# Kernel tuning notes

Hardware: AMD Instinct MI355X
Metric: run time of the kernel (lower is better)

Reference implementation:

```python
import jax, jax.numpy as jnp
import numpy as np

B, S, D, H = 4, 1024, 1024, 16
DH = D // H
K_SPARSE = 32
LAMBDA_MAX, ALPHA = 10.0, 5.0
SPARSE_THRESHOLD = 1.0


def setup_inputs() -> dict:
    key = jax.random.key(0)
    ks = jax.random.split(key, 12)
    x = jax.random.normal(ks[0], (B, S, D), dtype=jnp.float32)
    prior_mask = jax.random.bernoulli(ks[1], 0.1, (S, S))
    prior_indices = jax.random.randint(ks[2], (S, K_SPARSE), 0, S)
    prior_index_mask = jax.random.bernoulli(ks[3], 0.9, (S, K_SPARSE))
    prior_index_mask = prior_index_mask.at[:, 0].set(True)  # avoid all-masked rows
    u_prev = jax.random.normal(ks[4], (B, 1), dtype=jnp.float32)
    sc = 1.0 / np.sqrt(D)
    Wq = jax.random.normal(ks[5], (D, D), dtype=jnp.float32) * sc
    Wk = jax.random.normal(ks[6], (D, D), dtype=jnp.float32) * sc
    Wv = jax.random.normal(ks[7], (D, D), dtype=jnp.float32) * sc
    Wo = jax.random.normal(ks[8], (D, D), dtype=jnp.float32) * sc
    bq = jnp.zeros((D,), jnp.float32)
    bk = jnp.zeros((D,), jnp.float32)
    bv = jnp.zeros((D,), jnp.float32)
    bo = jnp.zeros((D,), jnp.float32)
    return {"x": x, "prior_mask": prior_mask, "prior_indices": prior_indices,
            "prior_index_mask": prior_index_mask, "u_prev": u_prev,
            "Wq": Wq, "bq": bq, "Wk": Wk, "bk": bk, "Wv": Wv, "bv": bv,
            "Wo": Wo, "bo": bo}


def reference(x, prior_mask, prior_indices, prior_index_mask, u_prev,
              Wq, bq, Wk, bk, Wv, bv, Wo, bo):
    Bb, Ss, Dd = x.shape
    scale = 1.0 / jnp.sqrt(jnp.asarray(DH, x.dtype))

    def proj(W, b):
        return (x @ W.T + b).reshape(Bb, Ss, H, DH).transpose(0, 2, 1, 3)  # [B,H,S,DH]

    Q, K, V = proj(Wq, bq), proj(Wk, bk), proj(Wv, bv)

    lam = LAMBDA_MAX * jnp.exp(-ALPHA * u_prev.reshape(Bb))  # [B]
    use_sparse = lam >= SPARSE_THRESHOLD                      # [B] bool

    # ---- dense branch: full SDPA with lambda-scaled prior bias ----
    scores = jnp.einsum('bhqd,bhkd->bhqk', Q, K) * scale      # [B,H,S,S]
    prior_bias = jnp.where(prior_mask[:Ss, :Ss], 0.0, -1.0).astype(x.dtype)
    bias = lam[:, None, None, None] * prior_bias[None, None]
    dense_out = jnp.einsum('bhqk,bhkd->bhqd',
                           jax.nn.softmax(scores + bias, axis=-1), V)

    # ---- sparse branch: gather-indexed SDPA over prior_indices ----
    idx = prior_indices[:Ss]                                   # [S,k]
    Kg = K[:, :, idx]                                          # [B,H,S,k,DH]
    Vg = V[:, :, idx]
    s_scores = jnp.einsum('bhsd,bhskd->bhsk', Q, Kg) * scale   # [B,H,S,k]
    s_scores = jnp.where(prior_index_mask[:Ss][None, None], s_scores,
                         jnp.asarray(-jnp.inf, x.dtype))
    sparse_out = jnp.einsum('bhsk,bhskd->bhsd',
                            jax.nn.softmax(s_scores, axis=-1), Vg)

    out = jnp.where(use_sparse[:, None, None, None], sparse_out, dense_out)
    out = out.transpose(0, 2, 1, 3).reshape(Bb, Ss, Dd)
    return out @ Wo.T + bo
```

## Files before the change

### kernel.cpp

```cpp
#include <hip/hip_runtime.h>
#include <hip/hip_bf16.h>
#include <cmath>

#define NB 4
#define NS 1024
#define ND 1024
#define NH 16
#define NDH 64
#define NKSP 32
#define SCALE 0.125f
#define LOG2E 1.44269504f
#define SCALE2 (SCALE * LOG2E)

typedef __attribute__((ext_vector_type(8))) short bf16x8;
typedef __attribute__((ext_vector_type(4))) float f32x4;
typedef unsigned long long u64;

#define AS1 __attribute__((address_space(1)))
#define AS3 __attribute__((address_space(3)))

__device__ __forceinline__ void gl_lds16(const void* g, void* l) {
    __builtin_amdgcn_global_load_lds((const AS1 void*)g, (AS3 void*)l, 16, 0, 0);
}

__device__ __forceinline__ ushort f2bf(float f) {
    union { __hip_bfloat16 h; ushort u; } cv;
    cv.h = __float2bfloat16(f);
    return cv.u;
}
__device__ __forceinline__ float bf2f(ushort u) {
    union { unsigned int i; float f; } cv;
    cv.i = ((unsigned int)u) << 16;
    return cv.f;
}
__device__ __forceinline__ float fexp2(float x) {
    return __builtin_amdgcn_exp2f(x);
}

__global__ __launch_bounds__(256)
void f2bf_multi(const float* __restrict__ x,
                const float* __restrict__ w0, const float* __restrict__ w1,
                const float* __restrict__ w2, const float* __restrict__ w3,
                const int* __restrict__ pm,
                ushort* __restrict__ xo,
                ushort* __restrict__ o0, ushort* __restrict__ o1,
                ushort* __restrict__ o2, ushort* __restrict__ o3,
                u64* __restrict__ bm)
{
    int y = blockIdx.y;
    if (y == 5) {
        int word = blockIdx.x * 4 + (threadIdx.x >> 6);
        int lane = threadIdx.x & 63;
        int row  = word >> 4, wcol = word & 15;
        int v = pm[(size_t)row * NS + wcol * 64 + lane];
        u64 b = __ballot(v != 0);
        if (lane == 0) bm[word] = b;
        return;
    }
    const float* src; ushort* dst; int nblk;
    if (y == 0)      { src = x;  dst = xo; nblk = 4096; }
    else if (y == 1) { src = w0; dst = o0; nblk = 1024; }
    else if (y == 2) { src = w1; dst = o1; nblk = 1024; }
    else if (y == 3) { src = w2; dst = o2; nblk = 1024; }
    else             { src = w3; dst = o3; nblk = 1024; }
    if (blockIdx.x >= (unsigned)nblk) return;
    int i = (blockIdx.x * 256 + threadIdx.x) * 4;
    float4 v = *(const float4*)&src[i];
    ushort4 o;
    o.x = f2bf(v.x); o.y = f2bf(v.y); o.z = f2bf(v.z); o.w = f2bf(v.w);
    *(ushort4*)&dst[i] = o;
}

__global__ __launch_bounds__(256)
void gemm_qkv(const ushort* __restrict__ xb,
              const ushort* __restrict__ Wqb, const ushort* __restrict__ Wkb,
              const ushort* __restrict__ Wvb,
              const float* __restrict__ bq, const float* __restrict__ bk,
              const float* __restrict__ bv,
              ushort* __restrict__ Qo, ushort* __restrict__ Ko,
              ushort* __restrict__ Vo)
{
    constexpr int K = ND;
    __shared__ __attribute__((aligned(16))) ushort As[128 * 32];
    __shared__ __attribute__((aligned(16))) ushort Bs[128 * 32];

    const int tid  = threadIdx.x;
    const int lane = tid & 63, w = tid >> 6;
    const int wm = w >> 1, wn = w & 1;
    const int which = blockIdx.x >> 3;
    const int n0 = (blockIdx.x & 7) * 128;
    const int m0 = blockIdx.y * 128;
    const int quad = lane >> 4, l16 = lane & 15;

    const ushort* W = (which == 0) ? Wqb : (which == 1) ? Wkb : Wvb;
    const float* bias = (which == 0) ? bq : (which == 1) ? bk : bv;
    ushort* Out = (which == 0) ? Qo : (which == 1) ? Ko : Vo;

    f32x4 acc[4][4] = {};

    for (int k0 = 0; k0 < K; k0 += 32) {
        __syncthreads();
#pragma unroll
        for (int u = 0; u < 2; ++u) {
            int t0 = u * 256 + w * 64;
            int t  = t0 + lane;
            int c  = t ^ ((t >> 3) & 7);
            int row = c >> 2, kc = (c & 3) * 8;
            gl_lds16(xb + (size_t)(m0 + row) * K + k0 + kc, &As[t0 * 8]);
            gl_lds16(W  + (size_t)(n0 + row) * K + k0 + kc, &Bs[t0 * 8]);
        }
        __syncthreads();

        bf16x8 af[4], bfr[4];
#pragma unroll
        for (int mt = 0; mt < 4; ++mt) {
            int cidx = (wm*64 + mt*16 + l16)*4 + quad;
            int p = cidx ^ ((cidx >> 3) & 7);
            af[mt] = *(const bf16x8*)&As[p * 8];
        }
#pragma unroll
        for (int nt = 0; nt < 4; ++nt) {
            int cidx = (wn*64 + nt*16 + l16)*4 + quad;
            int p = cidx ^ ((cidx >> 3) & 7);
            bfr[nt] = *(const bf16x8*)&Bs[p * 8];
        }
#pragma unroll
        for (int mt = 0; mt < 4; ++mt)
#pragma unroll
            for (int nt = 0; nt < 4; ++nt)
                acc[mt][nt] = __builtin_amdgcn_mfma_f32_16x16x32_bf16(
                    af[mt], bfr[nt], acc[mt][nt], 0, 0, 0);
    }

#pragma unroll
    for (int nt = 0; nt < 4; ++nt) {
        int n = n0 + wn*64 + nt*16 + l16;
        float bz = bias[n];
        int hh = n >> 6, dh = n & 63;
#pragma unroll
        for (int mt = 0; mt < 4; ++mt) {
#pragma unroll
            for (int rg = 0; rg < 4; ++rg) {
                int m = m0 + wm*64 + mt*16 + quad*4 + rg;
                int b = m >> 10, s = m & (NS - 1);
                Out[(((size_t)(b*NH + hh))*NS + s)*NDH + dh] =
                    f2bf(acc[mt][nt][rg] + bz);
            }
        }
    }
}

__global__ __launch_bounds__(256)
void transpose_v(const ushort* __restrict__ V, ushort* __restrict__ Vt)
{
    __shared__ __attribute__((aligned(16))) ushort T[64 * 64];

    const int t  = threadIdx.x;
    const int bh = blockIdx.x >> 4;
    const int st = blockIdx.x & 15;
    const ushort* Vh  = V  + (size_t)bh * NS * NDH + (size_t)st * 64 * NDH;
    ushort*       Vth = Vt + (size_t)bh * NDH * NS + st * 64;

#pragma unroll
    for (int i = 0; i < 2; ++i) {
        int g = i * 256 + t;
        int srow = g >> 3, sub = g & 7;
        union { bf16x8 v; ushort u[8]; } x;
        x.v = *(const bf16x8*)&Vh[(size_t)srow * NDH + sub * 8];
#pragma unroll
        for (int e = 0; e < 8; ++e) {
            int dh = sub * 8 + e;
            T[dh*64 + (((srow >> 3) ^ sub) * 8) + (srow & 7)] = x.u[e];
        }
    }
    __syncthreads();
#pragma unroll
    for (int i = 0; i < 2; ++i) {
        int g = i * 256 + t;
        int dh = g >> 3, sc = g & 7;
        bf16x8 v = *(const bf16x8*)&T[dh*64 + ((sc ^ (dh >> 3)) * 8)];
        *(bf16x8*)&Vth[(size_t)dh * NS + sc * 8] = v;
    }
}

__global__ __launch_bounds__(256)
void gemm_out(const ushort* __restrict__ A, const ushort* __restrict__ W,
              const float* __restrict__ bias, float* __restrict__ Cout)
{
    constexpr int K = ND;
    __shared__ __attribute__((aligned(16))) ushort As[64 * 32];
    __shared__ __attribute__((aligned(16))) ushort Bs[128 * 32];

    const int tid  = threadIdx.x;
    const int lane = tid & 63, w = tid >> 6;
    const int wm = w & 1, wn = w >> 1;
    const int m0 = blockIdx.y * 64, n0 = blockIdx.x * 128;
    const int quad = lane >> 4, l16 = lane & 15;

    f32x4 acc[2][4] = {};

    for (int k0 = 0; k0 < K; k0 += 32) {
        __syncthreads();
        {
            int t0 = w * 64;
            int t  = t0 + lane;
            int c  = t ^ ((t >> 3) & 7);
            int row = c >> 2, kc = (c & 3) * 8;
            gl_lds16(A + (size_t)(m0 + row) * K + k0 + kc, &As[t0 * 8]);
        }
#pragma unroll
        for (int u = 0; u < 2; ++u) {
            int t0 = u * 256 + w * 64;
            int t  = t0 + lane;
            int c  = t ^ ((t >> 3) & 7);
            int row = c >> 2, kc = (c & 3) * 8;
            gl_lds16(W + (size_t)(n0 + row) * K + k0 + kc, &Bs[t0 * 8]);
        }
        __syncthreads();

        bf16x8 af[2], bfr[4];
#pragma unroll
        for (int mt = 0; mt < 2; ++mt) {
            int cidx = (wm*32 + mt*16 + l16)*4 + quad;
            int p = cidx ^ ((cidx >> 3) & 7);
            af[mt] = *(const bf16x8*)&As[p * 8];
        }
#pragma unroll
        for (int nt = 0; nt < 4; ++nt) {
            int cidx = (wn*64 + nt*16 + l16)*4 + quad;
            int p = cidx ^ ((cidx >> 3) & 7);
            bfr[nt] = *(const bf16x8*)&Bs[p * 8];
        }
#pragma unroll
        for (int mt = 0; mt < 2; ++mt)
#pragma unroll
            for (int nt = 0; nt < 4; ++nt)
                acc[mt][nt] = __builtin_amdgcn_mfma_f32_16x16x32_bf16(
                    af[mt], bfr[nt], acc[mt][nt], 0, 0, 0);
    }

#pragma unroll
    for (int nt = 0; nt < 4; ++nt) {
        int n = n0 + wn*64 + nt*16 + l16;
        float bz = bias[n];
#pragma unroll
        for (int mt = 0; mt < 2; ++mt) {
#pragma unroll
            for (int rg = 0; rg < 4; ++rg) {
                int m = m0 + wm*32 + mt*16 + quad*4 + rg;
                Cout[(size_t)m * ND + n] = acc[mt][nt][rg] + bz;
            }
        }
    }
}

#define DSTAGE(T4)                                                            \
    _Pragma("unroll")                                                         \
    for (int u = 0; u < 8; ++u) {                                             \
        int cb = w * 512 + u * 64;                                            \
        int c  = cb + lane;                                                   \
        int tk = c >> 9, c2 = c & 511;                                        \
        int row = c2 >> 3, sub = c2 & 7;                                      \
        const ushort* src = Kh + (((size_t)(((T4)*4 + tk)*64 + row)) << 6)    \
                               + ((sub ^ (row & 7)) << 3);                    \
        gl_lds16(src, KK + (size_t)cb * 8);                                   \
    }

#define DLOADKV(KF, VF, KT)                                                   \
    _Pragma("unroll")                                                         \
    for (int nt = 0; nt < 4; ++nt)                                            \
        _Pragma("unroll")                                                     \
        for (int kk = 0; kk < 2; ++kk) {                                      \
            int rowk = nt*16 + l16;                                           \
            int ck = (kk*4 + quad) ^ (l16 & 7);                               \
            KF[nt][kk] = *(const bf16x8*)&KK[w*4096 + rowk*64 + ck*8];        \
            VF[nt][kk] = *(const bf16x8*)                                     \
                &Vth[(size_t)(nt*16 + l16) * NS + (KT)*64 + kk*32 + quad*8];  \
        }

#define DSTEP(KF, VF, M0, M1)                                                 \
    _Pragma("unroll")                                                         \
    for (int qh = 0; qh < 2; ++qh) {                                          \
        const int qrow = qh*16 + l16;                                         \
        u64 wqm = ((qh == 0) ? (M0) : (M1)) >> (quad * 4);                    \
        f32x4 s_acc[4] = {};                                                  \
        __builtin_amdgcn_s_setprio(1);                                        \
        _Pragma("unroll")                                                     \
        for (int nt = 0; nt < 4; ++nt)                                        \
            _Pragma("unroll")                                                 \
            for (int kk = 0; kk < 2; ++kk)                                    \
                s_acc[nt] = __builtin_amdgcn_mfma_f32_16x16x32_bf16(          \
                    KF[nt][kk], qf[qh][kk], s_acc[nt], 0, 0, 0);              \
        __builtin_amdgcn_s_setprio(0);                                        \
        _Pragma("unroll")                                                     \
        for (int nt = 0; nt < 4; ++nt) {                                      \
            ushort4 pk;                                                       \
            float p0 = fexp2(fmaf(s_acc[nt][0], SCALE2,                       \
                 ((wqm >> (nt*16 + 0)) & 1ULL) ? 0.f : nlam2));               \
            float p1 = fexp2(fmaf(s_acc[nt][1], SCALE2,                       \
                 ((wqm >> (nt*16 + 1)) & 1ULL) ? 0.f : nlam2));               \
            float p2 = fexp2(fmaf(s_acc[nt][2], SCALE2,                       \
                 ((wqm >> (nt*16 + 2)) & 1ULL) ? 0.f : nlam2));               \
            float p3 = fexp2(fmaf(s_acc[nt][3], SCALE2,                       \
                 ((wqm >> (nt*16 + 3)) & 1ULL) ? 0.f : nlam2));               \
            pk.x = f2bf(p0); pk.y = f2bf(p1);                                 \
            pk.z = f2bf(p2); pk.w = f2bf(p3);                                 \
            *(ushort4*)&Ps[w*2304 + qrow*72 + nt*16 + quad*4] = pk;           \
        }                                                                     \
        bf16x8 pf[2];                                                         \
        _Pragma("unroll")                                                     \
        for (int kk = 0; kk < 2; ++kk)                                        \
            pf[kk] = *(const bf16x8*)&Ps[w*2304 + qrow*72 + kk*32 + quad*8];  \
        __builtin_amdgcn_s_setprio(1);                                        \
        _Pragma("unroll")                                                     \
        for (int kk = 0; kk < 2; ++kk) {                                      \
            l_acc[qh] = __builtin_amdgcn_mfma_f32_16x16x32_bf16(              \
                pf[kk], ones.v, l_acc[qh], 0, 0, 0);                          \
            _Pragma("unroll")                                                 \
            for (int nt = 0; nt < 4; ++nt)                                    \
                o_acc[qh][nt] = __builtin_amdgcn_mfma_f32_16x16x32_bf16(      \
                    pf[kk], VF[nt][kk], o_acc[qh][nt], 0, 0, 0);              \
        }                                                                     \
        __builtin_amdgcn_s_setprio(0);                                        \
    }

__global__ __launch_bounds__(256)
void attn_dense(const ushort* __restrict__ Qb, const ushort* __restrict__ Kb,
                const ushort* __restrict__ Vt, const u64* __restrict__ bm,
                const float* __restrict__ u_prev, ushort* __restrict__ OA)
{
    __shared__ __attribute__((aligned(16))) ushort SM[25600];
    ushort* KK = SM;
    ushort* Ps = SM + 16384;

    const int tid  = threadIdx.x;
    const int lane = tid & 63, w = tid >> 6;
    const int quad = lane >> 4, l16 = lane & 15;

    float lams[4];
#pragma unroll
    for (int i = 0; i < 4; ++i) lams[i] = 10.0f * __expf(-5.0f * u_prev[i]);
    int dl[4], nd = 0;
#pragma unroll
    for (int i = 0; i < 4; ++i) if (lams[i] < 1.0f) dl[nd++] = i;

    const int id = blockIdx.x;
    if (id >= nd * 512) return;

    int xcd = id & 7, j = id >> 3;
    int nh2 = 2 * nd;
    int hi = j % nh2, qt = j / nh2;
    int gh = hi * 8 + xcd;
    const int b = dl[gh >> 4], h = gh & 15;
    const int s0 = qt * 32;
    const float nlam2 = -lams[b] * LOG2E;

    const size_t bh = (size_t)b * NH + h;
    const ushort* Qh  = Qb + bh * NS * NDH;
    const ushort* Kh  = Kb + bh * NS * NDH;
    const ushort* Vth = Vt + bh * NDH * NS;

    bf16x8 qf[2][2];
#pragma unroll
    for (int qh = 0; qh < 2; ++qh)
#pragma unroll
        for (int kk = 0; kk < 2; ++kk)
            qf[qh][kk] = *(const bf16x8*)
                &Qh[(size_t)(s0 + qh*16 + l16) * NDH + kk*32 + quad*8];

    union { bf16x8 v; ushort s[8]; } ones;
#pragma unroll
    for (int i = 0; i < 8; ++i) ones.s[i] = 0x3F80;

    f32x4 o_acc[2][4] = {};
    f32x4 l_acc[2] = {};

    for (int t = 0; t < 4; ++t) {
        if (t) __syncthreads();
        DSTAGE(t);
        const int kt = 4 * t + w;
        u64 m0 = bm[(size_t)(s0 +  0 + l16) * 16 + kt];
        u64 m1 = bm[(size_t)(s0 + 16 + l16) * 16 + kt];
        __syncthreads();
        bf16x8 kf[4][2], vf[4][2];
        DLOADKV(kf, vf, kt);
        DSTEP(kf, vf, m0, m1);
    }
    __syncthreads();

    float* POUT = (float*)SM;
    if (w != 0) {
        int base = (w - 1) * 2560;
#pragma unroll
        for (int qh = 0; qh < 2; ++qh) {
#pragma unroll
            for (int nt = 0; nt < 4; ++nt)
#pragma unroll
                for (int rg = 0; rg < 4; ++rg)
                    POUT[base + (qh*16 + nt*4 + rg)*64 + lane] =
                        o_acc[qh][nt][rg];
#pragma unroll
            for (int rg = 0; rg < 4; ++rg)
                POUT[base + (32 + qh*4 + rg)*64 + lane] = l_acc[qh][rg];
        }
    }
    __syncthreads();
    if (w == 0) {
#pragma unroll
        for (int s = 0; s < 3; ++s) {
            int base = s * 2560;
#pragma unroll
            for (int qh = 0; qh < 2; ++qh) {
#pragma unroll
                for (int nt = 0; nt < 4; ++nt)
#pragma unroll
                    for (int rg = 0; rg < 4; ++rg)
                        o_acc[qh][nt][rg] +=
                            POUT[base + (qh*16 + nt*4 + rg)*64 + lane];
#pragma unroll
                for (int rg = 0; rg < 4; ++rg)
                    l_acc[qh][rg] += POUT[base + (32 + qh*4 + rg)*64 + lane];
            }
        }
#pragma unroll
        for (int qh = 0; qh < 2; ++qh) {
            float inv[4];
#pragma unroll
            for (int rg = 0; rg < 4; ++rg) inv[rg] = 1.f / l_acc[qh][rg];
#pragma unroll
            for (int nt = 0; nt < 4; ++nt)
#pragma unroll
                for (int rg = 0; rg < 4; ++rg) {
                    int m = qh*16 + quad*4 + rg;
                    OA[((size_t)b*NS + s0 + m)*ND + h*NDH + nt*16 + l16] =
                        f2bf(o_acc[qh][nt][rg] * inv[rg]);
                }
        }
    }
}

__global__ __launch_bounds__(256)
void attn_sparse(const ushort* __restrict__ Qb, const ushort* __restrict__ Kb,
                 const ushort* __restrict__ Vb,
                 const int* __restrict__ pidx, const int* __restrict__ pimask,
                 const float* __restrict__ u_prev, ushort* __restrict__ OA)
{
    const int tid  = threadIdx.x;
    const int lane = tid & 63, w = tid >> 6;
    const int kj = lane >> 3;
    const int c  = lane & 7;

    float lams[4];
#pragma unroll
    for (int i = 0; i < 4; ++i) lams[i] = 10.0f * __expf(-5.0f * u_prev[i]);
    int sl[4], ns = 0;
#pragma unroll
    for (int i = 0; i < 4; ++i) if (lams[i] >= 1.0f) sl[ns++] = i;

    const int id = blockIdx.x;
    if (id >= ns * 1024) return;

    int xcd = id & 7, j = id >> 3;
    int nh2 = 2 * ns;
    int hi = j % nh2, qt = j / nh2;
    int gh = hi * 8 + xcd;
    const int b = sl[gh >> 4], h = gh & 15;
    const int s0 = qt * 16 + w * 4;

    const size_t bh = (size_t)b * NH + h;
    const ushort* Qh = Qb + bh * NS * NDH;
    const ushort* Kh = Kb + bh * NS * NDH;
    const ushort* Vh = Vb + bh * NS * NDH;

    for (int r = 0; r < 4; ++r) {
        const int s = s0 + r;

        float qf[8];
        {
            union { bf16x8 v; ushort u[8]; } qv;
            qv.v = *(const bf16x8*)&Qh[(size_t)s * NDH + c * 8];
#pragma unroll
            for (int e = 0; e < 8; ++e) qf[e] = bf2f(qv.u[e]);
        }

        int kv[4], mv[4];
#pragma unroll
        for (int jj = 0; jj < 4; ++jj) {
            kv[jj] = pidx  [(size_t)s * NKSP + jj*8 + kj];
            mv[jj] = pimask[(size_t)s * NKSP + jj*8 + kj];
        }

        float sc[4];
#pragma unroll
        for (int jj = 0; jj < 4; ++jj) {
            union { bf16x8 v; ushort u[8]; } kc8;
            kc8.v = *(const bf16x8*)&Kh[(size_t)kv[jj] * NDH + c * 8];
            float d = 0.f;
#pragma unroll
            for (int e = 0; e < 8; ++e) d = fmaf(qf[e], bf2f(kc8.u[e]), d);
            d += __shfl_xor(d, 1);
            d += __shfl_xor(d, 2);
            d += __shfl_xor(d, 4);
            sc[jj] = mv[jj] ? d * SCALE : -INFINITY;
        }

        float mt = fmaxf(fmaxf(sc[0], sc[1]), fmaxf(sc[2], sc[3]));
        mt = fmaxf(mt, __shfl_xor(mt, 8));
        mt = fmaxf(mt, __shfl_xor(mt, 16));
        mt = fmaxf(mt, __shfl_xor(mt, 32));

        float p[4], psum = 0.f;
#pragma unroll
        for (int jj = 0; jj < 4; ++jj) {
            p[jj] = __expf(sc[jj] - mt);
            psum += p[jj];
        }
        psum += __shfl_xor(psum, 8);
        psum += __shfl_xor(psum, 16);
        psum += __shfl_xor(psum, 32);

        float o[8];
#pragma unroll
        for (int e = 0; e < 8; ++e) o[e] = 0.f;
#pragma unroll
        for (int jj = 0; jj < 4; ++jj) {
            union { bf16x8 v; ushort u[8]; } vc8;
            vc8.v = *(const bf16x8*)&Vh[(size_t)kv[jj] * NDH + c * 8];
#pragma unroll
            for (int e = 0; e < 8; ++e)
                o[e] = fmaf(p[jj], bf2f(vc8.u[e]), o[e]);
        }
#pragma unroll
        for (int e = 0; e < 8; ++e) {
            o[e] += __shfl_xor(o[e], 8);
            o[e] += __shfl_xor(o[e], 16);
            o[e] += __shfl_xor(o[e], 32);
        }

        if (kj == 0) {
            float inv = 1.f / psum;
            union { bf16x8 v; ushort u[8]; } ov;
#pragma unroll
            for (int e = 0; e < 8; ++e) ov.u[e] = f2bf(o[e] * inv);
            *(bf16x8*)&OA[((size_t)b*NS + s)*ND + h*NDH + c*8] = ov.v;
        }
    }
}

extern "C" void kernel_launch(void* const* d_in, const int* in_sizes, int n_in,
                              void* d_out, int out_size, void* d_ws, size_t ws_size,
                              hipStream_t stream)
{
    const float* x      = (const float*)d_in[0];
    const int*   pmask  = (const int*)  d_in[1];
    const int*   pidx   = (const int*)  d_in[2];
    const int*   pimask = (const int*)  d_in[3];
    const float* u_prev = (const float*)d_in[4];
    const float* Wq     = (const float*)d_in[5];
    const float* bq     = (const float*)d_in[6];
    const float* Wk     = (const float*)d_in[7];
    const float* bk     = (const float*)d_in[8];
    const float* Wv     = (const float*)d_in[9];
    const float* bv     = (const float*)d_in[10];
    const float* Wo     = (const float*)d_in[11];
    const float* bo     = (const float*)d_in[12];
    float* out = (float*)d_out;

    const size_t QSZ = (size_t)NB * NH * NS * NDH;
    const size_t WSZ = (size_t)ND * ND;
    ushort* xb  = (ushort*)d_ws;
    ushort* Qw  = xb  + QSZ;
    ushort* Kw  = Qw  + QSZ;
    ushort* Vw  = Kw  + QSZ;
    ushort* Vtw = Vw  + QSZ;
    ushort* Awb = Vtw + QSZ;
    ushort* Wqb = Awb + QSZ;
    ushort* Wkb = Wqb + WSZ;
    ushort* Wvb = Wkb + WSZ;
    ushort* Wob = Wvb + WSZ;
    u64*    bmw = (u64*)(Wob + WSZ);

    f2bf_multi<<<dim3(4096, 6), 256, 0, stream>>>(
        x, Wq, Wk, Wv, Wo, pmask, xb, Wqb, Wkb, Wvb, Wob, bmw);

    gemm_qkv<<<dim3(24, 32), 256, 0, stream>>>(
        xb, Wqb, Wkb, Wvb, bq, bk, bv, Qw, Kw, Vw);

    transpose_v<<<1024, 256, 0, stream>>>(Vw, Vtw);

    attn_dense<<<2048, 256, 0, stream>>>(
        Qw, Kw, Vtw, bmw, u_prev, Awb);

    attn_sparse<<<4096, 256, 0, stream>>>(
        Qw, Kw, Vw, pidx, pimask, u_prev, Awb);

    gemm_out<<<dim3(ND/128, (NB*NS)/64), 256, 0, stream>>>(Awb, Wob, bo, out);
}
```

Before: 203.9 us.

## Fuse dense and sparse attention kernels into one launch with direct K loads

Merges the dense and sparse attention kernels into a single launch, with blocks dispatched by index into the dense or sparse branch according to each batch's lambda. The dense path stops staging K through LDS via async global-to-LDS copies and loads K fragments straight from global memory. It also shrinks shared memory by reducing partial results through one small buffer, one wave at a time. The goal is to remove a kernel launch and its tail, and to raise occupancy through lower LDS use. The cost is uncoalesced K reads from global memory and more barriers in the reduction.

```diff
diff --git a/kernel.cpp b/kernel.cpp
--- a/kernel.cpp
+++ b/kernel.cpp
@@ -254,26 +254,13 @@
     }
 }
 
-#define DSTAGE(T4)                                                            \
-    _Pragma("unroll")                                                         \
-    for (int u = 0; u < 8; ++u) {                                             \
-        int cb = w * 512 + u * 64;                                            \
-        int c  = cb + lane;                                                   \
-        int tk = c >> 9, c2 = c & 511;                                        \
-        int row = c2 >> 3, sub = c2 & 7;                                      \
-        const ushort* src = Kh + (((size_t)(((T4)*4 + tk)*64 + row)) << 6)    \
-                               + ((sub ^ (row & 7)) << 3);                    \
-        gl_lds16(src, KK + (size_t)cb * 8);                                   \
-    }
-
-#define DLOADKV(KF, VF, KT)                                                   \
+#define FLOADKV(KF, VF, KT)                                                   \
     _Pragma("unroll")                                                         \
     for (int nt = 0; nt < 4; ++nt)                                            \
         _Pragma("unroll")                                                     \
         for (int kk = 0; kk < 2; ++kk) {                                      \
-            int rowk = nt*16 + l16;                                           \
-            int ck = (kk*4 + quad) ^ (l16 & 7);                               \
-            KF[nt][kk] = *(const bf16x8*)&KK[w*4096 + rowk*64 + ck*8];        \
+            KF[nt][kk] = *(const bf16x8*)                                     \
+                &Kh[(size_t)((KT)*64 + nt*16 + l16) * NDH + kk*32 + quad*8];  \
             VF[nt][kk] = *(const bf16x8*)                                     \
                 &Vth[(size_t)(nt*16 + l16) * NS + (KT)*64 + kk*32 + quad*8];  \
         }
@@ -325,13 +312,14 @@
     }
 
 __global__ __launch_bounds__(256)
-void attn_dense(const ushort* __restrict__ Qb, const ushort* __restrict__ Kb,
-                const ushort* __restrict__ Vt, const u64* __restrict__ bm,
+void attn_fused(const ushort* __restrict__ Qb, const ushort* __restrict__ Kb,
+                const ushort* __restrict__ Vb, const ushort* __restrict__ Vt,
+                const u64* __restrict__ bm,
+                const int* __restrict__ pidx, const int* __restrict__ pimask,
                 const float* __restrict__ u_prev, ushort* __restrict__ OA)
 {
-    __shared__ __attribute__((aligned(16))) ushort SM[25600];
-    ushort* KK = SM;
-    ushort* Ps = SM + 16384;
+    __shared__ __attribute__((aligned(16))) ushort SM[9216];
+    ushort* Ps = SM;
 
     const int tid  = threadIdx.x;
     const int lane = tid & 63, w = tid >> 6;
@@ -340,209 +328,194 @@
     float lams[4];
 #pragma unroll
     for (int i = 0; i < 4; ++i) lams[i] = 10.0f * __expf(-5.0f * u_prev[i]);
-    int dl[4], nd = 0;
-#pragma unroll
-    for (int i = 0; i < 4; ++i) if (lams[i] < 1.0f) dl[nd++] = i;
+    int dl[4], sl[4], nd = 0, ns = 0;
+#pragma unroll
+    for (int i = 0; i < 4; ++i) if (lams[i] <  1.0f) dl[nd++] = i;
+#pragma unroll
+    for (int i = 0; i < 4; ++i) if (lams[i] >= 1.0f) sl[ns++] = i;
 
     const int id = blockIdx.x;
-    if (id >= nd * 512) return;
-
-    int xcd = id & 7, j = id >> 3;
-    int nh2 = 2 * nd;
-    int hi = j % nh2, qt = j / nh2;
-    int gh = hi * 8 + xcd;
-    const int b = dl[gh >> 4], h = gh & 15;
-    const int s0 = qt * 32;
-    const float nlam2 = -lams[b] * LOG2E;
-
-    const size_t bh = (size_t)b * NH + h;
-    const ushort* Qh  = Qb + bh * NS * NDH;
-    const ushort* Kh  = Kb + bh * NS * NDH;
-    const ushort* Vth = Vt + bh * NDH * NS;
-
-    bf16x8 qf[2][2];
-#pragma unroll
-    for (int qh = 0; qh < 2; ++qh)
-#pragma unroll
-        for (int kk = 0; kk < 2; ++kk)
-            qf[qh][kk] = *(const bf16x8*)
-                &Qh[(size_t)(s0 + qh*16 + l16) * NDH + kk*32 + quad*8];
-
-    union { bf16x8 v; ushort s[8]; } ones;
-#pragma unroll
-    for (int i = 0; i < 8; ++i) ones.s[i] = 0x3F80;
-
-    f32x4 o_acc[2][4] = {};
-    f32x4 l_acc[2] = {};
-
-    for (int t = 0; t < 4; ++t) {
-        if (t) __syncthreads();
-        DSTAGE(t);
-        const int kt = 4 * t + w;
-        u64 m0 = bm[(size_t)(s0 +  0 + l16) * 16 + kt];
-        u64 m1 = bm[(size_t)(s0 + 16 + l16) * 16 + kt];
+
+    if (id < nd * 512) {
+        int xcd = id & 7, j = id >> 3;
+        int nh2 = 2 * nd;
+        int hi = j % nh2, qt = j / nh2;
+        int gh = hi * 8 + xcd;
+        const int b = dl[gh >> 4], h = gh & 15;
+        const int s0 = qt * 32;
+        const float nlam2 = -lams[b] * LOG2E;
+
+        const size_t bh = (size_t)b * NH + h;
+        const ushort* Qh  = Qb + bh * NS * NDH;
+        const ushort* Kh  = Kb + bh * NS * NDH;
+        const ushort* Vth = Vt + bh * NDH * NS;
+
+        bf16x8 qf[2][2];
+#pragma unroll
+        for (int qh = 0; qh < 2; ++qh)
+#pragma unroll
+            for (int kk = 0; kk < 2; ++kk)
+                qf[qh][kk] = *(const bf16x8*)
+                    &Qh[(size_t)(s0 + qh*16 + l16) * NDH + kk*32 + quad*8];
+
+        union { bf16x8 v; ushort s[8]; } ones;
+#pragma unroll
+        for (int i = 0; i < 8; ++i) ones.s[i] = 0x3F80;
+
+        f32x4 o_acc[2][4] = {};
+        f32x4 l_acc[2] = {};
+
+        for (int t = 0; t < 4; ++t) {
+            const int kt = 4 * t + w;
+            u64 m0 = bm[(size_t)(s0 +  0 + l16) * 16 + kt];
+            u64 m1 = bm[(size_t)(s0 + 16 + l16) * 16 + kt];
+            bf16x8 kf[4][2], vf[4][2];
+            FLOADKV(kf, vf, kt);
+            DSTEP(kf, vf, m0, m1);
+        }
         __syncthreads();
-        bf16x8 kf[4][2], vf[4][2];
-        DLOADKV(kf, vf, kt);
-        DSTEP(kf, vf, m0, m1);
-    }
-    __syncthreads();
-
-    float* POUT = (float*)SM;
-    if (w != 0) {
-        int base = (w - 1) * 2560;
-#pragma unroll
-        for (int qh = 0; qh < 2; ++qh) {
-#pragma unroll
-            for (int nt = 0; nt < 4; ++nt)
-#pragma unroll
-                for (int rg = 0; rg < 4; ++rg)
-                    POUT[base + (qh*16 + nt*4 + rg)*64 + lane] =
-                        o_acc[qh][nt][rg];
-#pragma unroll
-            for (int rg = 0; rg < 4; ++rg)
-                POUT[base + (32 + qh*4 + rg)*64 + lane] = l_acc[qh][rg];
-        }
-    }
-    __syncthreads();
-    if (w == 0) {
-#pragma unroll
-        for (int s = 0; s < 3; ++s) {
-            int base = s * 2560;
+
+        float* POUT = (float*)SM;
+        for (int s = 1; s <= 3; ++s) {
+            if (w == s) {
+#pragma unroll
+                for (int qh = 0; qh < 2; ++qh) {
+#pragma unroll
+                    for (int nt = 0; nt < 4; ++nt)
+#pragma unroll
+                        for (int rg = 0; rg < 4; ++rg)
+                            POUT[(qh*16 + nt*4 + rg)*64 + lane] =
+                                o_acc[qh][nt][rg];
+#pragma unroll
+                    for (int rg = 0; rg < 4; ++rg)
+                        POUT[(32 + qh*4 + rg)*64 + lane] = l_acc[qh][rg];
+                }
+            }
+            __syncthreads();
+            if (w == 0) {
+#pragma unroll
+                for (int qh = 0; qh < 2; ++qh) {
+#pragma unroll
+                    for (int nt = 0; nt < 4; ++nt)
+#pragma unroll
+                        for (int rg = 0; rg < 4; ++rg)
+                            o_acc[qh][nt][rg] +=
+                                POUT[(qh*16 + nt*4 + rg)*64 + lane];
+#pragma unroll
+                    for (int rg = 0; rg < 4; ++rg)
+                        l_acc[qh][rg] += POUT[(32 + qh*4 + rg)*64 + lane];
+                }
+            }
+            __syncthreads();
+        }
+
+        if (w == 0) {
 #pragma unroll
             for (int qh = 0; qh < 2; ++qh) {
+                float inv[4];
+#pragma unroll
+                for (int rg = 0; rg < 4; ++rg) inv[rg] = 1.f / l_acc[qh][rg];
 #pragma unroll
                 for (int nt = 0; nt < 4; ++nt)
 #pragma unroll
-                    for (int rg = 0; rg < 4; ++rg)
-                        o_acc[qh][nt][rg] +=
-                            POUT[base + (qh*16 + nt*4 + rg)*64 + lane];
-#pragma unroll
-                for (int rg = 0; rg < 4; ++rg)
-                    l_acc[qh][rg] += POUT[base + (32 + qh*4 + rg)*64 + lane];
-            }
-        }
-#pragma unroll
-        for (int qh = 0; qh < 2; ++qh) {
-            float inv[4];
-#pragma unroll
-            for (int rg = 0; rg < 4; ++rg) inv[rg] = 1.f / l_acc[qh][rg];
-#pragma unroll
-            for (int nt = 0; nt < 4; ++nt)
-#pragma unroll
-                for (int rg = 0; rg < 4; ++rg) {
-                    int m = qh*16 + quad*4 + rg;
-                    OA[((size_t)b*NS + s0 + m)*ND + h*NDH + nt*16 + l16] =
-                        f2bf(o_acc[qh][nt][rg] * inv[rg]);
-                }
-        }
-    }
-}
-
-__global__ __launch_bounds__(256)
-void attn_sparse(const ushort* __restrict__ Qb, const ushort* __restrict__ Kb,
-                 const ushort* __restrict__ Vb,
-                 const int* __restrict__ pidx, const int* __restrict__ pimask,
-                 const float* __restrict__ u_prev, ushort* __restrict__ OA)
-{
-    const int tid  = threadIdx.x;
-    const int lane = tid & 63, w = tid >> 6;
-    const int kj = lane >> 3;
-    const int c  = lane & 7;
-
-    float lams[4];
-#pragma unroll
-    for (int i = 0; i < 4; ++i) lams[i] = 10.0f * __expf(-5.0f * u_prev[i]);
-    int sl[4], ns = 0;
-#pragma unroll
-    for (int i = 0; i < 4; ++i) if (lams[i] >= 1.0f) sl[ns++] = i;
-
-    const int id = blockIdx.x;
-    if (id >= ns * 1024) return;
-
-    int xcd = id & 7, j = id >> 3;
-    int nh2 = 2 * ns;
-    int hi = j % nh2, qt = j / nh2;
-    int gh = hi * 8 + xcd;
-    const int b = sl[gh >> 4], h = gh & 15;
-    const int s0 = qt * 16 + w * 4;
-
-    const size_t bh = (size_t)b * NH + h;
-    const ushort* Qh = Qb + bh * NS * NDH;
-    const ushort* Kh = Kb + bh * NS * NDH;
-    const ushort* Vh = Vb + bh * NS * NDH;
-
-    for (int r = 0; r < 4; ++r) {
-        const int s = s0 + r;
-
-        float qf[8];
-        {
-            union { bf16x8 v; ushort u[8]; } qv;
-            qv.v = *(const bf16x8*)&Qh[(size_t)s * NDH + c * 8];
-#pragma unroll
-            for (int e = 0; e < 8; ++e) qf[e] = bf2f(qv.u[e]);
-        }
-
-        int kv[4], mv[4];
-#pragma unroll
-        for (int jj = 0; jj < 4; ++jj) {
-            kv[jj] = pidx  [(size_t)s * NKSP + jj*8 + kj];
-            mv[jj] = pimask[(size_t)s * NKSP + jj*8 + kj];
-        }
-
-        float sc[4];
-#pragma unroll
-        for (int jj = 0; jj < 4; ++jj) {
-            union { bf16x8 v; ushort u[8]; } kc8;
-            kc8.v = *(const bf16x8*)&Kh[(size_t)kv[jj] * NDH + c * 8];
-            float d = 0.f;
-#pragma unroll
-            for (int e = 0; e < 8; ++e) d = fmaf(qf[e], bf2f(kc8.u[e]), d);
-            d += __shfl_xor(d, 1);
-            d += __shfl_xor(d, 2);
-            d += __shfl_xor(d, 4);
-            sc[jj] = mv[jj] ? d * SCALE : -INFINITY;
-        }
-
-        float mt = fmaxf(fmaxf(sc[0], sc[1]), fmaxf(sc[2], sc[3]));
-        mt = fmaxf(mt, __shfl_xor(mt, 8));
-        mt = fmaxf(mt, __shfl_xor(mt, 16));
-        mt = fmaxf(mt, __shfl_xor(mt, 32));
-
-        float p[4], psum = 0.f;
-#pragma unroll
-        for (int jj = 0; jj < 4; ++jj) {
-            p[jj] = __expf(sc[jj] - mt);
-            psum += p[jj];
-        }
-        psum += __shfl_xor(psum, 8);
-        psum += __shfl_xor(psum, 16);
-        psum += __shfl_xor(psum, 32);
-
-        float o[8];
-#pragma unroll
-        for (int e = 0; e < 8; ++e) o[e] = 0.f;
-#pragma unroll
-        for (int jj = 0; jj < 4; ++jj) {
-            union { bf16x8 v; ushort u[8]; } vc8;
-            vc8.v = *(const bf16x8*)&Vh[(size_t)kv[jj] * NDH + c * 8];
-#pragma unroll
-            for (int e = 0; e < 8; ++e)
-                o[e] = fmaf(p[jj], bf2f(vc8.u[e]), o[e]);
-        }
-#pragma unroll
-        for (int e = 0; e < 8; ++e) {
-            o[e] += __shfl_xor(o[e], 8);
-            o[e] += __shfl_xor(o[e], 16);
-            o[e] += __shfl_xor(o[e], 32);
-        }
-
-        if (kj == 0) {
-            float inv = 1.f / psum;
-            union { bf16x8 v; ushort u[8]; } ov;
-#pragma unroll
-            for (int e = 0; e < 8; ++e) ov.u[e] = f2bf(o[e] * inv);
-            *(bf16x8*)&OA[((size_t)b*NS + s)*ND + h*NDH + c*8] = ov.v;
+                    for (int rg = 0; rg < 4; ++rg) {
+                        int m = qh*16 + quad*4 + rg;
+                        OA[((size_t)b*NS + s0 + m)*ND + h*NDH + nt*16 + l16] =
+                            f2bf(o_acc[qh][nt][rg] * inv[rg]);
+                    }
+            }
+        }
+    } else {
+        const int sid = id - nd * 512;
+        if (sid >= ns * 1024) return;
+
+        const int kj = lane >> 3;
+        const int c  = lane & 7;
+
+        int xcd = sid & 7, j = sid >> 3;
+        int nh2 = 2 * ns;
+        int hi = j % nh2, qt = j / nh2;
+        int gh = hi * 8 + xcd;
+        const int b = sl[gh >> 4], h = gh & 15;
+        const int s0 = qt * 16 + w * 4;
+
+        const size_t bh = (size_t)b * NH + h;
+        const ushort* Qh = Qb + bh * NS * NDH;
+        const ushort* Kh = Kb + bh * NS * NDH;
+        const ushort* Vh = Vb + bh * NS * NDH;
+
+        for (int r = 0; r < 4; ++r) {
+            const int s = s0 + r;
+
+            float qf[8];
+            {
+                union { bf16x8 v; ushort u[8]; } qv;
+                qv.v = *(const bf16x8*)&Qh[(size_t)s * NDH + c * 8];
+#pragma unroll
+                for (int e = 0; e < 8; ++e) qf[e] = bf2f(qv.u[e]);
+            }
+
+            int kv[4], mv[4];
+#pragma unroll
+            for (int jj = 0; jj < 4; ++jj) {
+                kv[jj] = pidx  [(size_t)s * NKSP + jj*8 + kj];
+                mv[jj] = pimask[(size_t)s * NKSP + jj*8 + kj];
+            }
+
+            float sc[4];
+#pragma unroll
+            for (int jj = 0; jj < 4; ++jj) {
+                union { bf16x8 v; ushort u[8]; } kc8;
+                kc8.v = *(const bf16x8*)&Kh[(size_t)kv[jj] * NDH + c * 8];
+                float d = 0.f;
+#pragma unroll
+                for (int e = 0; e < 8; ++e) d = fmaf(qf[e], bf2f(kc8.u[e]), d);
+                d += __shfl_xor(d, 1);
+                d += __shfl_xor(d, 2);
+                d += __shfl_xor(d, 4);
+                sc[jj] = mv[jj] ? d * SCALE : -INFINITY;
+            }
+
+            float mt = fmaxf(fmaxf(sc[0], sc[1]), fmaxf(sc[2], sc[3]));
+            mt = fmaxf(mt, __shfl_xor(mt, 8));
+            mt = fmaxf(mt, __shfl_xor(mt, 16));
+            mt = fmaxf(mt, __shfl_xor(mt, 32));
+
+            float p[4], psum = 0.f;
+#pragma unroll
+            for (int jj = 0; jj < 4; ++jj) {
+                p[jj] = __expf(sc[jj] - mt);
+                psum += p[jj];
+            }
+            psum += __shfl_xor(psum, 8);
+            psum += __shfl_xor(psum, 16);
+            psum += __shfl_xor(psum, 32);
+
+            float o[8];
+#pragma unroll
+            for (int e = 0; e < 8; ++e) o[e] = 0.f;
+#pragma unroll
+            for (int jj = 0; jj < 4; ++jj) {
+                union { bf16x8 v; ushort u[8]; } vc8;
+                vc8.v = *(const bf16x8*)&Vh[(size_t)kv[jj] * NDH + c * 8];
+#pragma unroll
+                for (int e = 0; e < 8; ++e)
+                    o[e] = fmaf(p[jj], bf2f(vc8.u[e]), o[e]);
+            }
+#pragma unroll
+            for (int e = 0; e < 8; ++e) {
+                o[e] += __shfl_xor(o[e], 8);
+                o[e] += __shfl_xor(o[e], 16);
+                o[e] += __shfl_xor(o[e], 32);
+            }
+
+            if (kj == 0) {
+                float inv = 1.f / psum;
+                union { bf16x8 v; ushort u[8]; } ov;
+#pragma unroll
+                for (int e = 0; e < 8; ++e) ov.u[e] = f2bf(o[e] * inv);
+                *(bf16x8*)&OA[((size_t)b*NS + s)*ND + h*NDH + c*8] = ov.v;
+            }
         }
     }
 }
@@ -588,11 +561,8 @@
 
     transpose_v<<<1024, 256, 0, stream>>>(Vw, Vtw);
 
-    attn_dense<<<2048, 256, 0, stream>>>(
-        Qw, Kw, Vtw, bmw, u_prev, Awb);
-
-    attn_sparse<<<4096, 256, 0, stream>>>(
-        Qw, Kw, Vw, pidx, pimask, u_prev, Awb);
+    attn_fused<<<4096, 256, 0, stream>>>(
+        Qw, Kw, Vw, Vtw, bmw, pidx, pimask, u_prev, Awb);
 
     gemm_out<<<dim3(ND/128, (NB*NS)/64), 256, 0, stream>>>(Awb, Wob, bo, out);
 }
```

After: 221.4 us. 1.09x slower.
